# Performance work log

Measured on AMD Instinct MI355X. Metric: run time of the kernel, lower is better.

Reference implementation:

```python
import jax, jax.numpy as jnp
import numpy as np

B, T, DIM, R, H = 8, 512, 512, 2048, 8
HD = DIM // H
FFH = int(DIM * 2.66)  # 1362, matches int(dim*2.66) in HybridForwardBlock
BETA, SFA_INC, TAU_SFA = 0.95, 0.05, 20.0
EPS = 1e-6


def ternary(w):
    # TernarySTE: quantize forward, identity gradient (STE)
    thr = jnp.abs(w).mean() * 0.7
    q = (jnp.abs(w) > thr).astype(w.dtype) * jnp.sign(w)
    return w + jax.lax.stop_gradient(q - w)


@jax.custom_vjp
def spike_fn(m):
    return (m > 0).astype(m.dtype)

def _spike_fwd(m):
    return spike_fn(m), m

def _spike_bwd(m, g):
    return (g * (1.0 - jnp.tanh(m) ** 2) * 0.5,)

spike_fn.defvjp(_spike_fwd, _spike_bwd)


def rmsnorm(x, w):
    return x * jax.lax.rsqrt(jnp.mean(x * x, axis=-1, keepdims=True) + EPS) * w


def setup_inputs() -> dict:
    key = jax.random.key(0)
    ks = jax.random.split(key, 16)
    def W(k, shape, fan_in):
        return (jax.random.normal(k, shape, jnp.float32) / np.float32(np.sqrt(fan_in)))
    return {
        "x": jax.random.normal(ks[0], (B, T, DIM), jnp.float32),
        "Wi": W(ks[1], (R, DIM), DIM),           # input_proj
        "bi": jnp.zeros((R,), jnp.float32),
        "Wr": W(ks[2], (R, R), R),               # recurrent_proj (no bias)
        "rn_w": jnp.ones((R,), jnp.float32),     # readout_norm
        "W1": W(ks[3], (2 * DIM, R), R),         # readout_mlp layer 1
        "b1": jnp.zeros((2 * DIM,), jnp.float32),
        "W2": W(ks[4], (DIM, 2 * DIM), 2 * DIM), # readout_mlp layer 2
        "b2": jnp.zeros((DIM,), jnp.float32),
        "anorm_w": jnp.ones((DIM,), jnp.float32),
        "Wqkv": W(ks[5], (3 * DIM, DIM), DIM),
        "Wo": W(ks[6], (DIM, DIM), DIM),
        "fnorm_w": jnp.ones((DIM,), jnp.float32),
        "Wf1": W(ks[7], (FFH, DIM), DIM),
        "Wf2": W(ks[8], (DIM, FFH), FFH),
        "Wf3": W(ks[9], (FFH, DIM), DIM),
        "beta": jnp.full((R,), BETA, jnp.float32),        # LIF buffers (non-trainable)
        "sfa_inc": jnp.full((R,), SFA_INC, jnp.float32),
        "sfa_decay": jnp.full((R,), float(np.exp(-1.0 / TAU_SFA)), jnp.float32),
    }


def reference(x, Wi, bi, Wr, rn_w, W1, b1, W2, b2, anorm_w, Wqkv, Wo, fnorm_w,
              Wf1, Wf2, Wf3, beta, sfa_inc, sfa_decay):
    # ---- GatedLSM: spiking LIF reservoir scan over time ----
    xp = jnp.einsum('btd,rd->btr', x, ternary(Wi)) + bi   # precompute input current [B,T,R]
    Wr_q = ternary(Wr)

    def step(carry, xt):
        mem, ath, last = carry
        cur = xt + last @ Wr_q.T                          # total_current [B,R]
        mem = beta * mem + cur
        spk = spike_fn(mem - (1.0 + ath))                 # initial_threshold + adaptive_th
        mem = mem * (1.0 - jax.lax.stop_gradient(spk))    # reset (spike detached)
        ath = sfa_decay * ath + sfa_inc * spk
        return (mem, ath, spk), spk

    z = jnp.zeros((B, R), x.dtype)
    (_, _, _), spikes = jax.lax.scan(step, (z, z, z), jnp.swapaxes(xp, 0, 1))
    acts = jnp.swapaxes(spikes, 0, 1)                     # [B,T,R]

    # readout: RMSNorm -> Linear -> GELU -> Linear (dropout off in eval)
    hn = rmsnorm(acts, rn_w)
    h = jax.nn.gelu(jnp.einsum('btr,hr->bth', hn, ternary(W1)) + b1, approximate=False)
    y = jnp.einsum('bth,dh->btd', h, ternary(W2)) + b2    # [B,T,DIM]

    # ---- Gated attention readout block (residual attn + SwiGLU FFN) ----
    xa = rmsnorm(y, anorm_w)
    qkv = jnp.einsum('btd,ed->bte', xa, ternary(Wqkv))
    q, k, v = jnp.split(qkv, 3, axis=-1)
    def heads(t):
        return t.reshape(B, T, H, HD).transpose(0, 2, 1, 3)  # [B,H,T,HD]
    q, k, v = heads(q), heads(k), heads(v)
    scores = jnp.einsum('bhqd,bhkd->bhqk', q, k) * (HD ** -0.5)
    attn = jax.nn.softmax(scores, axis=-1)
    o = jnp.einsum('bhqk,bhkd->bhqd', attn, v).transpose(0, 2, 1, 3).reshape(B, T, DIM)
    x_res = y + jnp.einsum('btd,ed->bte', o, ternary(Wo))

    xf = rmsnorm(x_res, fnorm_w)
    g = jax.nn.silu(jnp.einsum('btd,hd->bth', xf, ternary(Wf1)))
    u = jnp.einsum('btd,hd->bth', xf, ternary(Wf3))
    x_out = x_res + jnp.einsum('bth,dh->btd', g * u, ternary(Wf2))
    return x_out
```

## Files before the change

kernel.cpp:

```cpp
#include <hip/hip_runtime.h>
#include <stdint.h>

typedef unsigned int u32;
typedef unsigned long long u64;

#define CB 8
#define CT 512
#define CDIM 512
#define CR 2048
#define CH 8
#define CHD 64
#define CFFMAX 1368
#define CM 4096
#define SCAN_WGS 64

__global__ __launch_bounds__(256) void k_abssum(const float* __restrict__ w, long n,
                                                double* __restrict__ sums, int idx){
  double s = 0.0;
  long stride = (long)gridDim.x * blockDim.x;
  for (long i = (long)blockIdx.x*blockDim.x + threadIdx.x; i < n; i += stride)
    s += (double)fabsf(w[i]);
  #pragma unroll
  for (int d = 32; d; d >>= 1) s += __shfl_down(s, d);
  __shared__ double ps[4];
  int lane = threadIdx.x & 63, wv = threadIdx.x >> 6;
  if (lane == 0) ps[wv] = s;
  __syncthreads();
  if (threadIdx.x == 0) atomicAdd(&sums[idx], ps[0]+ps[1]+ps[2]+ps[3]);
}

__global__ __launch_bounds__(256) void k_decode(const float* __restrict__ w, float* __restrict__ q,
                                                long n, const double* __restrict__ sums, int idx, double invN){
  double thr = 0.7 * (sums[idx] * invN);
  long stride = (long)gridDim.x * blockDim.x;
  for (long i = (long)blockIdx.x*blockDim.x + threadIdx.x; i < n; i += stride){
    float v = w[i];
    q[i] = (fabs((double)v) > thr) ? (v > 0.0f ? 1.0f : -1.0f) : 0.0f;
  }
}

__global__ __launch_bounds__(256) void k_decodeT(const float* __restrict__ w, float* __restrict__ qT,
                                                 long rows, long cols, const double* __restrict__ sums,
                                                 int idx, double invN){
  double thr = 0.7 * (sums[idx] * invN);
  long n = rows * cols;
  long stride = (long)gridDim.x * blockDim.x;
  for (long i = (long)blockIdx.x*blockDim.x + threadIdx.x; i < n; i += stride){
    long r = i / cols, d = i - r*cols;
    float v = w[i];
    float o = (fabs((double)v) > thr) ? (v > 0.0f ? 1.0f : -1.0f) : 0.0f;
    qT[d*rows + r] = o;
  }
}

__global__ __launch_bounds__(256) void k_xp(const float* __restrict__ x, const float* __restrict__ wiqT,
                                            const float* __restrict__ bi, double* __restrict__ xp){
  int t = blockIdx.y;
  int r = blockIdx.x*256 + threadIdx.x;
  __shared__ double xs[CB][CDIM];
  for (int i = threadIdx.x; i < CB*CDIM; i += 256){
    int b = i >> 9, d = i & 511;
    xs[b][d] = (double)x[((size_t)b*CT + t)*CDIM + d];
  }
  __syncthreads();
  double acc[CB];
  #pragma unroll
  for (int b = 0; b < CB; ++b) acc[b] = 0.0;
  for (int d = 0; d < CDIM; ++d){
    double wd = (double)wiqT[(size_t)d*CR + r];
    #pragma unroll
    for (int b = 0; b < CB; ++b) acc[b] = fma(wd, xs[b][d], acc[b]);
  }
  double bd = (double)bi[r];
  double* o = xp + ((size_t)t*CR + r)*CB;
  #pragma unroll
  for (int b = 0; b < CB; ++b) o[b] = acc[b] + bd;
}

__global__ __launch_bounds__(256) void k_scan(const float* __restrict__ Wr,
                                              const double* __restrict__ xp,
                                              const float* __restrict__ beta,
                                              const float* __restrict__ sfi,
                                              const float* __restrict__ sfd,
                                              const double* __restrict__ sums,
                                              u32* __restrict__ acts,
                                              u32* __restrict__ pub,
                                              u32* __restrict__ arrive){
  __shared__ u32 spk32[CB][64];
  __shared__ unsigned char sbyte[CB][32];
  int tid = threadIdx.x;
  int g = blockIdx.x;
  int rbase = g * 32;
  int row = tid >> 3, k = tid & 7;
  double thr = 0.7 * (sums[1] * (1.0/((double)CR*(double)CR)));
  u64 mpos[4], mneg[4];
  #pragma unroll
  for (int j = 0; j < 4; ++j){
    int w = k + 8*j;
    const float* wr = Wr + ((size_t)(rbase+row))*CR + w*64;
    u64 pos = 0, neg = 0;
    for (int jj = 0; jj < 64; jj += 4){
      float4 v4 = *reinterpret_cast<const float4*>(wr + jj);
      float vv[4] = {v4.x, v4.y, v4.z, v4.w};
      #pragma unroll
      for (int c = 0; c < 4; ++c){
        if (fabs((double)vv[c]) > thr){
          if (vv[c] > 0.0f) pos |= (1ull << (jj + c));
          else              neg |= (1ull << (jj + c));
        }
      }
    }
    mpos[j] = pos; mneg[j] = neg;
  }
  spk32[tid >> 6][tid & 63] = 0;
  spk32[(tid >> 6) + 4][tid & 63] = 0;
  int r = rbase + row;
  double mem = 0.0, ath = 0.0;
  double bt = (double)beta[r], dc = (double)sfd[r], ic = (double)sfi[r];
  const double* xpr = xp + (size_t)r*CB + k;
  __syncthreads();
  double xv = xpr[0];
  for (int t = 0; t < CT; ++t){
    double xv_next = (t+1 < CT) ? xpr[(size_t)(t+1)*CR*CB] : 0.0;
    int pa[8] = {0,0,0,0,0,0,0,0};
    int na[8] = {0,0,0,0,0,0,0,0};
    #pragma unroll
    for (int j = 0; j < 4; ++j){
      int w = k + 8*j;
      #pragma unroll
      for (int b = 0; b < CB; ++b){
        u64 s = *reinterpret_cast<const u64*>(&spk32[b][2*w]);
        pa[b] += __popcll(s & mpos[j]);
        na[b] += __popcll(s & mneg[j]);
      }
    }
    int rec[8];
    #pragma unroll
    for (int b = 0; b < CB; ++b) rec[b] = pa[b] - na[b];
    #pragma unroll
    for (int b = 0; b < CB; ++b) rec[b] += __shfl_xor(rec[b], 1);
    #pragma unroll
    for (int b = 0; b < CB; ++b) rec[b] += __shfl_xor(rec[b], 2);
    #pragma unroll
    for (int b = 0; b < CB; ++b) rec[b] += __shfl_xor(rec[b], 4);
    double cur = xv + (double)rec[k];
    mem = bt*mem + cur;
    bool sp = (mem - (1.0 + ath)) > 0.0;
    mem = sp ? 0.0 : mem;
    ath = dc*ath + (sp ? ic : 0.0);
    sbyte[k][row] = sp ? (unsigned char)1 : (unsigned char)0;
    xv = xv_next;
    __syncthreads();
    if (tid < CB){
      const u32* sb = reinterpret_cast<const u32*>(&sbyte[tid][0]);
      u32 word = 0;
      #pragma unroll
      for (int i = 0; i < 8; ++i){
        u32 wv = sb[i];
        word |= ((wv & 1u) | ((wv >> 7) & 2u) | ((wv >> 14) & 4u) | ((wv >> 21) & 8u)) << (4*i);
      }
      acts[((size_t)tid*CT + t)*64 + g] = word;
      pub[(((size_t)(t+1)&1)*CB + tid)*64 + g] = word;
    }
    if (tid == 0)
      __hip_atomic_store(&arrive[(size_t)g*32], (u32)(t+1),
                         __ATOMIC_RELEASE, __HIP_MEMORY_SCOPE_AGENT);
    if (t+1 < CT){
      if (tid < 64){
        while (__hip_atomic_load(&arrive[(size_t)tid*32], __ATOMIC_ACQUIRE,
                                 __HIP_MEMORY_SCOPE_AGENT) < (u32)(t+1)) { }
      }
      __syncthreads();
      int par = (t+1) & 1;
      int b0 = tid >> 6, g0 = tid & 63;
      spk32[b0][g0]     = pub[((size_t)par*CB + b0)*64 + g0];
      spk32[b0 + 4][g0] = pub[((size_t)par*CB + b0 + 4)*64 + g0];
      __syncthreads();
    }
  }
}

__global__ __launch_bounds__(256) void k_hn(const u32* __restrict__ acts, const float* __restrict__ rn_w,
                                            float* __restrict__ hn){
  int rowbt = blockIdx.x;
  int b = rowbt >> 9, t = rowbt & 511;
  __shared__ u32 wlds[64];
  __shared__ int pc[64];
  __shared__ float sS;
  int tid = threadIdx.x;
  const u32* src = acts + ((size_t)b*CT + t)*64;
  if (tid < 64){ u32 w = src[tid]; wlds[tid] = w; pc[tid] = __popc(w); }
  __syncthreads();
  if (tid == 0){
    int c = 0;
    for (int i = 0; i < 64; ++i) c += pc[i];
    sS = 1.0f / sqrtf((float)c * (1.0f/(float)CR) + 1e-6f);
  }
  __syncthreads();
  float s = sS;
  #pragma unroll
  for (int i = 0; i < 8; ++i){
    int r = tid + 256*i;
    u32 w = wlds[r >> 5];
    float v = ((w >> (r & 31)) & 1u) ? s * rn_w[r] : 0.0f;
    hn[(size_t)rowbt*CR + r] = v;
  }
}

struct GemmP {
  const float* A; long lda, Ab, Ah;
  const float* B; long ldb, Bb, Bh;
  float* C;       long ldc, Cb, Ch;
  const float* bias;
  const float* res; long ldr, Rb, Rh;
  float scale;
  int M, N, K, HH;
};

template<int EPI, bool BT>
__global__ __launch_bounds__(256) void k_gemm(GemmP p){
  int bz = blockIdx.z;
  int bb = bz / p.HH, hh = bz - bb*p.HH;
  const float* A = p.A + (size_t)bb*p.Ab + (size_t)hh*p.Ah;
  const float* B = p.B + (size_t)bb*p.Bb + (size_t)hh*p.Bh;
  float* C = p.C + (size_t)bb*p.Cb + (size_t)hh*p.Ch;
  const float* R = p.res ? (p.res + (size_t)bb*p.Rb + (size_t)hh*p.Rh) : (const float*)0;
  int m0 = blockIdx.y*128, n0 = blockIdx.x*128;
  __shared__ float As[16][132];
  __shared__ float Bs[16][132];
  int tid = threadIdx.x;
  int tx = tid & 15, ty = tid >> 4;
  bool a4 = ((p.lda & 3) == 0);
  bool b4 = ((p.ldb & 3) == 0);
  float acc[8][8];
  #pragma unroll
  for (int i = 0; i < 8; ++i)
    #pragma unroll
    for (int j = 0; j < 8; ++j) acc[i][j] = 0.0f;
  for (int k0 = 0; k0 < p.K; k0 += 16){
    {
      int mr = tid >> 2, kc = (tid & 3)*4;
      #pragma unroll
      for (int ps = 0; ps < 2; ++ps){
        int mm = mr + ps*64, gm = m0 + mm, gk = k0 + kc;
        float4 v = make_float4(0.f,0.f,0.f,0.f);
        if (gm < p.M){
          if (a4 && (gk + 3 < p.K)) v = *reinterpret_cast<const float4*>(&A[(size_t)gm*p.lda + gk]);
          else {
            float tv[4];
            #pragma unroll
            for (int c = 0; c < 4; ++c) tv[c] = (gk+c < p.K) ? A[(size_t)gm*p.lda + gk + c] : 0.0f;
            v = make_float4(tv[0],tv[1],tv[2],tv[3]);
          }
        }
        As[kc+0][mm] = v.x; As[kc+1][mm] = v.y; As[kc+2][mm] = v.z; As[kc+3][mm] = v.w;
      }
    }
    if (BT){
      int nr = tid >> 2, kc = (tid & 3)*4;
      #pragma unroll
      for (int ps = 0; ps < 2; ++ps){
        int nn = nr + ps*64, gn = n0 + nn, gk = k0 + kc;
        float4 v = make_float4(0.f,0.f,0.f,0.f);
        if (gn < p.N){
          if (b4 && (gk + 3 < p.K)) v = *reinterpret_cast<const float4*>(&B[(size_t)gn*p.ldb + gk]);
          else {
            float tv[4];
            #pragma unroll
            for (int c = 0; c < 4; ++c) tv[c] = (gk+c < p.K) ? B[(size_t)gn*p.ldb + gk + c] : 0.0f;
            v = make_float4(tv[0],tv[1],tv[2],tv[3]);
          }
        }
        Bs[kc+0][nn] = v.x; Bs[kc+1][nn] = v.y; Bs[kc+2][nn] = v.z; Bs[kc+3][nn] = v.w;
      }
    } else {
      int kr = tid >> 5, nc = (tid & 31)*4;
      #pragma unroll
      for (int ps = 0; ps < 2; ++ps){
        int kk = kr + ps*8, gk = k0 + kk, gn = n0 + nc;
        float4 v = make_float4(0.f,0.f,0.f,0.f);
        if (gk < p.K){
          if (b4 && (gn + 3 < p.N)) v = *reinterpret_cast<const float4*>(&B[(size_t)gk*p.ldb + gn]);
          else {
            float tv[4];
            #pragma unroll
            for (int c = 0; c < 4; ++c) tv[c] = (gn+c < p.N) ? B[(size_t)gk*p.ldb + gn + c] : 0.0f;
            v = make_float4(tv[0],tv[1],tv[2],tv[3]);
          }
        }
        *reinterpret_cast<float4*>(&Bs[kk][nc]) = v;
      }
    }
    __syncthreads();
    #pragma unroll
    for (int kk = 0; kk < 16; ++kk){
      float a[8], b[8];
      *reinterpret_cast<float4*>(&a[0]) = *reinterpret_cast<const float4*>(&As[kk][ty*8]);
      *reinterpret_cast<float4*>(&a[4]) = *reinterpret_cast<const float4*>(&As[kk][ty*8+4]);
      *reinterpret_cast<float4*>(&b[0]) = *reinterpret_cast<const float4*>(&Bs[kk][tx*8]);
      *reinterpret_cast<float4*>(&b[4]) = *reinterpret_cast<const float4*>(&Bs[kk][tx*8+4]);
      #pragma unroll
      for (int i = 0; i < 8; ++i)
        #pragma unroll
        for (int j = 0; j < 8; ++j)
          acc[i][j] = fmaf(a[i], b[j], acc[i][j]);
    }
    __syncthreads();
  }
  #pragma unroll
  for (int i = 0; i < 8; ++i){
    int gm = m0 + ty*8 + i;
    if (gm >= p.M) continue;
    #pragma unroll
    for (int j = 0; j < 8; ++j){
      int gn = n0 + tx*8 + j;
      if (gn >= p.N) continue;
      float v = acc[i][j] * p.scale;
      if (EPI == 1){ v += p.bias[gn]; v = 0.5f*v*(1.0f + erff(v*0.7071067811865475f)); }
      else if (EPI == 2){ v += p.bias[gn]; }
      else if (EPI == 3){ v = v / (1.0f + expf(-v)); }
      else if (EPI == 4){ v += R[(size_t)gm*p.ldr + gn]; }
      C[(size_t)gm*p.ldc + gn] = v;
    }
  }
}

template<int EPI, bool BT>
static void run_gemm(const GemmP& p, hipStream_t s, int nbat){
  dim3 grid((p.N + 127)/128, (p.M + 127)/128, nbat), blk(256);
  k_gemm<EPI, BT><<<grid, blk, 0, s>>>(p);
}

__global__ __launch_bounds__(256) void k_softmax(float* __restrict__ sc, long rows){
  long gw = ((long)blockIdx.x*blockDim.x + threadIdx.x) >> 6;
  int lane = threadIdx.x & 63;
  if (gw >= rows) return;
  float* row = sc + gw*512;
  float4 v1 = *reinterpret_cast<const float4*>(row + lane*8);
  float4 v2 = *reinterpret_cast<const float4*>(row + lane*8 + 4);
  float v[8] = {v1.x, v1.y, v1.z, v1.w, v2.x, v2.y, v2.z, v2.w};
  float mx = v[0];
  #pragma unroll
  for (int e = 1; e < 8; ++e) mx = fmaxf(mx, v[e]);
  #pragma unroll
  for (int d = 32; d; d >>= 1) mx = fmaxf(mx, __shfl_xor(mx, d));
  float sum = 0.0f;
  #pragma unroll
  for (int e = 0; e < 8; ++e){ v[e] = expf(v[e] - mx); sum += v[e]; }
  #pragma unroll
  for (int d = 32; d; d >>= 1) sum += __shfl_xor(sum, d);
  float inv = 1.0f / sum;
  float4 o1 = make_float4(v[0]*inv, v[1]*inv, v[2]*inv, v[3]*inv);
  float4 o2 = make_float4(v[4]*inv, v[5]*inv, v[6]*inv, v[7]*inv);
  *reinterpret_cast<float4*>(row + lane*8) = o1;
  *reinterpret_cast<float4*>(row + lane*8 + 4) = o2;
}

__global__ __launch_bounds__(256) void k_rmsnorm(const float* __restrict__ x, const float* __restrict__ w,
                                                 float* __restrict__ o, long rows){
  long gw = ((long)blockIdx.x*blockDim.x + threadIdx.x) >> 6;
  int lane = threadIdx.x & 63;
  if (gw >= rows) return;
  const float* xr = x + gw*512;
  float v[8]; float ss = 0.0f;
  #pragma unroll
  for (int e = 0; e < 8; ++e){ v[e] = xr[lane*8 + e]; ss = fmaf(v[e], v[e], ss); }
  #pragma unroll
  for (int d = 32; d; d >>= 1) ss += __shfl_xor(ss, d);
  float r = 1.0f / sqrtf(ss*(1.0f/512.0f) + 1e-6f);
  float* orow = o + gw*512;
  #pragma unroll
  for (int e = 0; e < 8; ++e) orow[lane*8 + e] = v[e]*r*w[lane*8 + e];
}

__global__ __launch_bounds__(256) void k_mul(float* __restrict__ g, const float* __restrict__ u, long n){
  long stride = (long)gridDim.x * blockDim.x;
  for (long i = (long)blockIdx.x*blockDim.x + threadIdx.x; i < n; i += stride) g[i] *= u[i];
}

extern "C" void kernel_launch(void* const* d_in, const int* in_sizes, int n_in,
                              void* d_out, int out_size, void* d_ws, size_t ws_size,
                              hipStream_t stream){
  (void)n_in; (void)out_size;
  const float* x    = (const float*)d_in[0];
  const float* Wi   = (const float*)d_in[1];
  const float* bi   = (const float*)d_in[2];
  const float* Wr   = (const float*)d_in[3];
  const float* rn_w = (const float*)d_in[4];
  const float* W1   = (const float*)d_in[5];
  const float* b1   = (const float*)d_in[6];
  const float* W2   = (const float*)d_in[7];
  const float* b2   = (const float*)d_in[8];
  const float* anw  = (const float*)d_in[9];
  const float* Wqkv = (const float*)d_in[10];
  const float* Wo   = (const float*)d_in[11];
  const float* fnw  = (const float*)d_in[12];
  const float* Wf1  = (const float*)d_in[13];
  const float* Wf2  = (const float*)d_in[14];
  const float* Wf3  = (const float*)d_in[15];
  const float* beta = (const float*)d_in[16];
  const float* sfi  = (const float*)d_in[17];
  const float* sfd  = (const float*)d_in[18];

  const long FF = (long)in_sizes[13] / CDIM;

  char* ws = (char*)d_ws;
  size_t cur = 0;
  auto alloc = [&](size_t bytes){ size_t o = cur; cur += (bytes + 255) & ~(size_t)255; return o; };
  size_t oCTRL = alloc(16384);
  size_t oPUB  = alloc((size_t)2*CB*64*4);
  size_t oACTS = alloc((size_t)CB*CT*64*4);
  size_t oXP   = alloc((size_t)CT*CR*CB*8);
  size_t oWIQT = alloc((size_t)CDIM*CR*4);
  size_t oW1Q  = alloc((size_t)1024*CR*4);
  size_t oW2Q  = alloc((size_t)512*1024*4);
  size_t oWQKV = alloc((size_t)1536*512*4);
  size_t oWOQ  = alloc((size_t)512*512*4);
  size_t oWF1Q = alloc((size_t)CFFMAX*512*4);
  size_t oWF2Q = alloc((size_t)512*CFFMAX*4);
  size_t oWF3Q = alloc((size_t)CFFMAX*512*4);
  size_t oHN   = alloc((size_t)CM*CR*4);
  size_t oH    = alloc((size_t)CM*1024*4);
  size_t oY    = alloc((size_t)CM*512*4);
  size_t oXA   = alloc((size_t)CM*512*4);
  size_t oQKV  = alloc((size_t)CM*1536*4);
  size_t oO    = alloc((size_t)CM*512*4);
  size_t oXR   = alloc((size_t)CM*512*4);
  if (cur > ws_size) return;

  double* sums = (double*)(ws + oCTRL + 128);
  u32* arrive = (u32*)(ws + oCTRL + 4096);
  u32* pub = (u32*)(ws + oPUB);
  u32* uACTS = (u32*)(ws + oACTS);
  double* dXP = (double*)(ws + oXP);
  float* fSC  = (float*)(ws + oXP);
  float* fWIQT = (float*)(ws + oWIQT);
  float* fW1Q = (float*)(ws + oW1Q);
  float* fW2Q = (float*)(ws + oW2Q);
  float* fWQKV = (float*)(ws + oWQKV);
  float* fWOQ = (float*)(ws + oWOQ);
  float* fWF1Q = (float*)(ws + oWF1Q);
  float* fWF2Q = (float*)(ws + oWF2Q);
  float* fWF3Q = (float*)(ws + oWF3Q);
  float* fHN = (float*)(ws + oHN);
  float* fG  = (float*)(ws + oHN);
  float* fH  = (float*)(ws + oH);
  float* fY  = (float*)(ws + oY);
  float* fXA = (float*)(ws + oXA);
  float* fQKV = (float*)(ws + oQKV);
  float* fU  = (float*)(ws + oQKV);
  float* fO  = (float*)(ws + oO);
  float* fXR = (float*)(ws + oXR);
  float* out = (float*)d_out;

  dim3 b256(256);
  hipMemsetAsync(ws + oCTRL, 0, 16384, stream);

  k_abssum<<<512, b256, 0, stream>>>(Wi,  (long)CR*CDIM,  sums, 0);
  k_abssum<<<512, b256, 0, stream>>>(Wr,  (long)CR*CR,    sums, 1);
  k_abssum<<<512, b256, 0, stream>>>(W1,  (long)1024*CR,  sums, 2);
  k_abssum<<<512, b256, 0, stream>>>(W2,  (long)512*1024, sums, 3);
  k_abssum<<<512, b256, 0, stream>>>(Wqkv,(long)1536*512, sums, 4);
  k_abssum<<<512, b256, 0, stream>>>(Wo,  (long)512*512,  sums, 5);
  k_abssum<<<512, b256, 0, stream>>>(Wf1, FF*512,         sums, 6);
  k_abssum<<<512, b256, 0, stream>>>(Wf2, 512*FF,         sums, 7);
  k_abssum<<<512, b256, 0, stream>>>(Wf3, FF*512,         sums, 8);

  k_decodeT<<<1024, b256, 0, stream>>>(Wi, fWIQT, CR, CDIM, sums, 0, 1.0/((double)CR*CDIM));
  k_decode<<<1024, b256, 0, stream>>>(W1,  fW1Q, (long)1024*CR,  sums, 2, 1.0/((double)1024*CR));
  k_decode<<<1024, b256, 0, stream>>>(W2,  fW2Q, (long)512*1024, sums, 3, 1.0/((double)512*1024));
  k_decode<<<1024, b256, 0, stream>>>(Wqkv,fWQKV,(long)1536*512, sums, 4, 1.0/((double)1536*512));
  k_decode<<<1024, b256, 0, stream>>>(Wo,  fWOQ, (long)512*512,  sums, 5, 1.0/((double)512*512));
  k_decode<<<1024, b256, 0, stream>>>(Wf1, fWF1Q, FF*512,        sums, 6, 1.0/((double)FF*512));
  k_decode<<<1024, b256, 0, stream>>>(Wf2, fWF2Q, 512*FF,        sums, 7, 1.0/((double)FF*512));
  k_decode<<<1024, b256, 0, stream>>>(Wf3, fWF3Q, FF*512,        sums, 8, 1.0/((double)FF*512));

  k_xp<<<dim3(CR/256, CT), b256, 0, stream>>>(x, fWIQT, bi, dXP);
  k_scan<<<SCAN_WGS, b256, 0, stream>>>(Wr, dXP, beta, sfi, sfd, sums, uACTS, pub, arrive);
  k_hn<<<CM, b256, 0, stream>>>(uACTS, rn_w, fHN);

  { GemmP p{fHN, CR,0,0,  fW1Q, CR,0,0,  fH, 1024,0,0,  b1,  (const float*)0,0,0,0, 1.0f, CM,1024,CR,1};
    run_gemm<1,true>(p, stream, 1); }
  { GemmP p{fH, 1024,0,0, fW2Q, 1024,0,0, fY, 512,0,0,  b2,  (const float*)0,0,0,0, 1.0f, CM,512,1024,1};
    run_gemm<2,true>(p, stream, 1); }
  k_rmsnorm<<<CM/4, b256, 0, stream>>>(fY, anw, fXA, CM);
  { GemmP p{fXA, 512,0,0, fWQKV, 512,0,0, fQKV, 1536,0,0, (const float*)0, (const float*)0,0,0,0, 1.0f, CM,1536,512,1};
    run_gemm<0,true>(p, stream, 1); }
  { GemmP p{fQKV,       1536, 786432, 64,
            fQKV + 512, 1536, 786432, 64,
            fSC,        512,  2097152, 262144,
            (const float*)0, (const float*)0,0,0,0, 0.125f, 512,512,64,CH};
    run_gemm<0,true>(p, stream, CB*CH); }
  k_softmax<<<(long)CB*CH*512/4, b256, 0, stream>>>(fSC, (long)CB*CH*512);
  { GemmP p{fSC,         512,  2097152, 262144,
            fQKV + 1024, 1536, 786432,  64,
            fO,          512,  262144,  64,
            (const float*)0, (const float*)0,0,0,0, 1.0f, 512,64,512,CH};
    run_gemm<0,false>(p, stream, CB*CH); }
  { GemmP p{fO, 512,0,0, fWOQ, 512,0,0, fXR, 512,0,0, (const float*)0, fY, 512,0,0, 1.0f, CM,512,512,1};
    run_gemm<4,true>(p, stream, 1); }
  k_rmsnorm<<<CM/4, b256, 0, stream>>>(fXR, fnw, fXA, CM);
  { GemmP p{fXA, 512,0,0, fWF1Q, 512,0,0, fG, FF,0,0, (const float*)0, (const float*)0,0,0,0, 1.0f, CM,(int)FF,512,1};
    run_gemm<3,true>(p, stream, 1); }
  { GemmP p{fXA, 512,0,0, fWF3Q, 512,0,0, fU, FF,0,0, (const float*)0, (const float*)0,0,0,0, 1.0f, CM,(int)FF,512,1};
    run_gemm<0,true>(p, stream, 1); }
  k_mul<<<2048, b256, 0, stream>>>(fG, fU, (long)CM*FF);
  { GemmP p{fG, FF,0,0, fWF2Q, FF,0,0, out, 512,0,0, (const float*)0, fXR, 512,0,0, 1.0f, CM,512,(int)FF,1};
    run_gemm<4,true>(p, stream, 1); }
}
```

Before: 4.653 ms.

## Repartition spiking scan by batch groups with per-thread neuron masks

The recurrent scan is re-split so that each batch element is handled by its own group of 8 workgroups, and each thread owns a full neuron row with all 32 mask words held in registers. Spikes are packed with a wavefront ballot. Synchronisation now happens only among the 8 workgroups that share a batch element, through per-packet flags, replacing the previous all-64 barrier. Ternary mask construction moves into a separate precompute kernel, and the xp layout is changed to match the new access pattern. In exchange, each thread holds 64 u64 mask values, which raises register pressure.

```diff
diff --git a/kernel.cpp b/kernel.cpp
--- a/kernel.cpp
+++ b/kernel.cpp
@@ -12,7 +12,6 @@
 #define CHD 64
 #define CFFMAX 1368
 #define CM 4096
-#define SCAN_WGS 64
 
 __global__ __launch_bounds__(256) void k_abssum(const float* __restrict__ w, long n,
                                                 double* __restrict__ sums, int idx){
@@ -53,6 +52,29 @@
   }
 }
 
+__global__ __launch_bounds__(256) void k_maskbuild(const float* __restrict__ Wr,
+                                                   const double* __restrict__ sums,
+                                                   u64* __restrict__ mb){
+  int n = blockIdx.x*256 + threadIdx.x;
+  int r = n >> 5, w = n & 31;
+  double thr = 0.7 * (sums[1] * (1.0/((double)CR*(double)CR)));
+  const float* src = Wr + (size_t)r*CR + w*64;
+  u64 pos = 0, neg = 0;
+  for (int j = 0; j < 64; j += 4){
+    float4 v4 = *reinterpret_cast<const float4*>(src + j);
+    float vv[4] = {v4.x, v4.y, v4.z, v4.w};
+    #pragma unroll
+    for (int c = 0; c < 4; ++c){
+      if (fabs((double)vv[c]) > thr){
+        if (vv[c] > 0.0f) pos |= (1ull << (j + c));
+        else              neg |= (1ull << (j + c));
+      }
+    }
+  }
+  mb[((size_t)r*32 + w)*2 + 0] = pos;
+  mb[((size_t)r*32 + w)*2 + 1] = neg;
+}
+
 __global__ __launch_bounds__(256) void k_xp(const float* __restrict__ x, const float* __restrict__ wiqT,
                                             const float* __restrict__ bi, double* __restrict__ xp){
   int t = blockIdx.y;
@@ -72,109 +94,75 @@
     for (int b = 0; b < CB; ++b) acc[b] = fma(wd, xs[b][d], acc[b]);
   }
   double bd = (double)bi[r];
-  double* o = xp + ((size_t)t*CR + r)*CB;
-  #pragma unroll
-  for (int b = 0; b < CB; ++b) o[b] = acc[b] + bd;
-}
-
-__global__ __launch_bounds__(256) void k_scan(const float* __restrict__ Wr,
-                                              const double* __restrict__ xp,
-                                              const float* __restrict__ beta,
-                                              const float* __restrict__ sfi,
-                                              const float* __restrict__ sfd,
-                                              const double* __restrict__ sums,
-                                              u32* __restrict__ acts,
-                                              u32* __restrict__ pub,
-                                              u32* __restrict__ arrive){
-  __shared__ u32 spk32[CB][64];
-  __shared__ unsigned char sbyte[CB][32];
+  #pragma unroll
+  for (int b = 0; b < CB; ++b)
+    xp[((size_t)b*CT + t)*CR + r] = acc[b] + bd;
+}
+
+__global__ __launch_bounds__(256, 1) void k_scan(const u64* __restrict__ mb,
+                                                 const double* __restrict__ xp,
+                                                 const float* __restrict__ beta,
+                                                 const float* __restrict__ sfi,
+                                                 const float* __restrict__ sfd,
+                                                 u32* __restrict__ acts,
+                                                 u64* __restrict__ pub){
+  __shared__ u64 spk[32];
+  __shared__ u64 bal[4];
   int tid = threadIdx.x;
-  int g = blockIdx.x;
-  int rbase = g * 32;
-  int row = tid >> 3, k = tid & 7;
-  double thr = 0.7 * (sums[1] * (1.0/((double)CR*(double)CR)));
-  u64 mpos[4], mneg[4];
-  #pragma unroll
-  for (int j = 0; j < 4; ++j){
-    int w = k + 8*j;
-    const float* wr = Wr + ((size_t)(rbase+row))*CR + w*64;
-    u64 pos = 0, neg = 0;
-    for (int jj = 0; jj < 64; jj += 4){
-      float4 v4 = *reinterpret_cast<const float4*>(wr + jj);
-      float vv[4] = {v4.x, v4.y, v4.z, v4.w};
-      #pragma unroll
-      for (int c = 0; c < 4; ++c){
-        if (fabs((double)vv[c]) > thr){
-          if (vv[c] > 0.0f) pos |= (1ull << (jj + c));
-          else              neg |= (1ull << (jj + c));
-        }
-      }
-    }
-    mpos[j] = pos; mneg[j] = neg;
-  }
-  spk32[tid >> 6][tid & 63] = 0;
-  spk32[(tid >> 6) + 4][tid & 63] = 0;
-  int r = rbase + row;
+  int blk = blockIdx.x;
+  int x = blk & 7;
+  int wgin = blk >> 3;
+  int r = wgin*256 + tid;
+  u64 mpos[32], mneg[32];
+  const u64* m = mb + (size_t)r*64;
+  #pragma unroll
+  for (int w = 0; w < 32; ++w){ mpos[w] = m[2*w]; mneg[w] = m[2*w+1]; }
+  if (tid < 32) spk[tid] = 0;
   double mem = 0.0, ath = 0.0;
   double bt = (double)beta[r], dc = (double)sfd[r], ic = (double)sfi[r];
-  const double* xpr = xp + (size_t)r*CB + k;
+  const double* xpr = xp + ((size_t)x*CT)*CR + r;
   __syncthreads();
   double xv = xpr[0];
   for (int t = 0; t < CT; ++t){
-    double xv_next = (t+1 < CT) ? xpr[(size_t)(t+1)*CR*CB] : 0.0;
-    int pa[8] = {0,0,0,0,0,0,0,0};
-    int na[8] = {0,0,0,0,0,0,0,0};
-    #pragma unroll
-    for (int j = 0; j < 4; ++j){
-      int w = k + 8*j;
-      #pragma unroll
-      for (int b = 0; b < CB; ++b){
-        u64 s = *reinterpret_cast<const u64*>(&spk32[b][2*w]);
-        pa[b] += __popcll(s & mpos[j]);
-        na[b] += __popcll(s & mneg[j]);
-      }
-    }
-    int rec[8];
-    #pragma unroll
-    for (int b = 0; b < CB; ++b) rec[b] = pa[b] - na[b];
-    #pragma unroll
-    for (int b = 0; b < CB; ++b) rec[b] += __shfl_xor(rec[b], 1);
-    #pragma unroll
-    for (int b = 0; b < CB; ++b) rec[b] += __shfl_xor(rec[b], 2);
-    #pragma unroll
-    for (int b = 0; b < CB; ++b) rec[b] += __shfl_xor(rec[b], 4);
-    double cur = xv + (double)rec[k];
+    double xv_next = (t+1 < CT) ? xpr[(size_t)(t+1)*CR] : 0.0;
+    int pa = 0, na = 0;
+    #pragma unroll
+    for (int w = 0; w < 32; ++w){
+      u64 s = spk[w];
+      pa += __popcll(s & mpos[w]);
+      na += __popcll(s & mneg[w]);
+    }
+    double cur = xv + (double)(pa - na);
     mem = bt*mem + cur;
     bool sp = (mem - (1.0 + ath)) > 0.0;
     mem = sp ? 0.0 : mem;
     ath = dc*ath + (sp ? ic : 0.0);
-    sbyte[k][row] = sp ? (unsigned char)1 : (unsigned char)0;
+    u64 ball = __ballot(sp);
+    if ((tid & 63) == 0) bal[tid >> 6] = ball;
     xv = xv_next;
     __syncthreads();
-    if (tid < CB){
-      const u32* sb = reinterpret_cast<const u32*>(&sbyte[tid][0]);
-      u32 word = 0;
-      #pragma unroll
-      for (int i = 0; i < 8; ++i){
-        u32 wv = sb[i];
-        word |= ((wv & 1u) | ((wv >> 7) & 2u) | ((wv >> 14) & 4u) | ((wv >> 21) & 8u)) << (4*i);
-      }
-      acts[((size_t)tid*CT + t)*64 + g] = word;
-      pub[(((size_t)(t+1)&1)*CB + tid)*64 + g] = word;
-    }
-    if (tid == 0)
-      __hip_atomic_store(&arrive[(size_t)g*32], (u32)(t+1),
-                         __ATOMIC_RELEASE, __HIP_MEMORY_SCOPE_AGENT);
+    if (tid < 8){
+      u64 b64 = bal[tid >> 1];
+      u32 wrd = (u32)(b64 >> ((tid & 1)*32));
+      acts[((size_t)x*CT + t)*64 + wgin*8 + tid] = wrd;
+    }
     if (t+1 < CT){
-      if (tid < 64){
-        while (__hip_atomic_load(&arrive[(size_t)tid*32], __ATOMIC_ACQUIRE,
-                                 __HIP_MEMORY_SCOPE_AGENT) < (u32)(t+1)) { }
-      }
-      __syncthreads();
       int par = (t+1) & 1;
-      int b0 = tid >> 6, g0 = tid & 63;
-      spk32[b0][g0]     = pub[((size_t)par*CB + b0)*64 + g0];
-      spk32[b0 + 4][g0] = pub[((size_t)par*CB + b0 + 4)*64 + g0];
+      if (tid == 0){
+        u64* mypkt = pub + (((size_t)par*8 + x)*8 + wgin)*8;
+        mypkt[0] = bal[0]; mypkt[1] = bal[1]; mypkt[2] = bal[2]; mypkt[3] = bal[3];
+        __hip_atomic_store(&mypkt[4], (u64)(u32)(t+1),
+                           __ATOMIC_RELEASE, __HIP_MEMORY_SCOPE_AGENT);
+      }
+      if (tid < 8){
+        u64* pk = pub + (((size_t)par*8 + x)*8 + tid)*8;
+        while ((u32)__hip_atomic_load(&pk[4], __ATOMIC_ACQUIRE,
+                                      __HIP_MEMORY_SCOPE_AGENT) < (u32)(t+1)) { }
+        spk[tid*4 + 0] = pk[0];
+        spk[tid*4 + 1] = pk[1];
+        spk[tid*4 + 2] = pk[2];
+        spk[tid*4 + 3] = pk[3];
+      }
       __syncthreads();
     }
   }
@@ -408,7 +396,7 @@
   size_t cur = 0;
   auto alloc = [&](size_t bytes){ size_t o = cur; cur += (bytes + 255) & ~(size_t)255; return o; };
   size_t oCTRL = alloc(16384);
-  size_t oPUB  = alloc((size_t)2*CB*64*4);
+  size_t oMB   = alloc((size_t)CR*32*2*8);
   size_t oACTS = alloc((size_t)CB*CT*64*4);
   size_t oXP   = alloc((size_t)CT*CR*CB*8);
   size_t oWIQT = alloc((size_t)CDIM*CR*4);
@@ -429,8 +417,8 @@
   if (cur > ws_size) return;
 
   double* sums = (double*)(ws + oCTRL + 128);
-  u32* arrive = (u32*)(ws + oCTRL + 4096);
-  u32* pub = (u32*)(ws + oPUB);
+  u64* pub = (u64*)(ws + oCTRL + 8192);
+  u64* uMB = (u64*)(ws + oMB);
   u32* uACTS = (u32*)(ws + oACTS);
   double* dXP = (double*)(ws + oXP);
   float* fSC  = (float*)(ws + oXP);
@@ -466,6 +454,7 @@
   k_abssum<<<512, b256, 0, stream>>>(Wf2, 512*FF,         sums, 7);
   k_abssum<<<512, b256, 0, stream>>>(Wf3, FF*512,         sums, 8);
 
+  k_maskbuild<<<256, b256, 0, stream>>>(Wr, sums, uMB);
   k_decodeT<<<1024, b256, 0, stream>>>(Wi, fWIQT, CR, CDIM, sums, 0, 1.0/((double)CR*CDIM));
   k_decode<<<1024, b256, 0, stream>>>(W1,  fW1Q, (long)1024*CR,  sums, 2, 1.0/((double)1024*CR));
   k_decode<<<1024, b256, 0, stream>>>(W2,  fW2Q, (long)512*1024, sums, 3, 1.0/((double)512*1024));
@@ -476,7 +465,7 @@
   k_decode<<<1024, b256, 0, stream>>>(Wf3, fWF3Q, FF*512,        sums, 8, 1.0/((double)FF*512));
 
   k_xp<<<dim3(CR/256, CT), b256, 0, stream>>>(x, fWIQT, bi, dXP);
-  k_scan<<<SCAN_WGS, b256, 0, stream>>>(Wr, dXP, beta, sfi, sfd, sums, uACTS, pub, arrive);
+  k_scan<<<64, b256, 0, stream>>>(uMB, dXP, beta, sfi, sfd, uACTS, pub);
   k_hn<<<CM, b256, 0, stream>>>(uACTS, rn_w, fHN);
 
   { GemmP p{fHN, CR,0,0,  fW1Q, CR,0,0,  fH, 1024,0,0,  b1,  (const float*)0,0,0,0, 1.0f, CM,1024,CR,1};
```

Result: faster. 3.776 ms (-18.8%).
